# Kernel optimization log

Measured on AMD Instinct MI355X. Metric: run time of the kernel, lower is better.

## Reference

```python
import jax, jax.numpy as jnp
import numpy as np

EPSILON = 0.3
ALPHA = 0.7
LN_EPS = 1e-5


def _layernorm(x, g, b):
    mu = jnp.mean(x, axis=-1, keepdims=True)
    var = jnp.mean((x - mu) ** 2, axis=-1, keepdims=True)
    return (x - mu) / jnp.sqrt(var + LN_EPS) * g + b


def setup_inputs() -> dict:
    key = jax.random.key(0)
    ks = jax.random.split(key, 6)
    B, N, D, L = 1, 2048, 768, 16
    s = 0.05  # weight scale to keep sigmoid/exp well-conditioned
    return {
        "x": jax.random.normal(ks[0], (B, N, D), jnp.float32),
        "proj_w": jax.random.normal(ks[1], (D, L), jnp.float32) * s,
        "proj_b": jnp.zeros((L,), jnp.float32),
        "ln1_g": jnp.ones((L,), jnp.float32),
        "ln1_b": jnp.zeros((L,), jnp.float32),
        "pi_w1": jax.random.normal(ks[2], (L, D), jnp.float32) * s,
        "pi_b1": jnp.zeros((D,), jnp.float32),
        "pi_w2": jax.random.normal(ks[3], (D, 1), jnp.float32) * s,
        "pi_b2": jnp.zeros((1,), jnp.float32),
        "dt": jnp.full((1,), 0.05, jnp.float32),
        "f_w": jax.random.normal(ks[4], (D, D), jnp.float32) * s,
        "f_b": jnp.zeros((D,), jnp.float32),
        "ln2_g": jnp.ones((D,), jnp.float32),
        "ln2_b": jnp.zeros((D,), jnp.float32),
    }


def reference(x, proj_w, proj_b, ln1_g, ln1_b, pi_w1, pi_b1, pi_w2, pi_b2, dt, f_w, f_b, ln2_g, ln2_b):
    B, N, D = x.shape
    # proj_list: Linear -> LayerNorm -> ReLU. [B,N,L]
    x_proj = jax.nn.relu(_layernorm(x @ proj_w + proj_b, ln1_g, ln1_b))
    # RBF kernel over pairwise differences. [B,N,N]
    diff = x_proj[:, :, None, :] - x_proj[:, None, :, :]
    K_eps = jnp.exp(-(1.0 / (4.0 * EPSILON)) * jnp.sum(diff * diff, axis=-1))
    q_tilde = jnp.sum(K_eps, axis=2)  # [B,N]
    # pi_list: Linear -> ReLU -> Linear -> Sigmoid. [B,N]
    pi = jax.nn.sigmoid(jax.nn.relu(x_proj @ pi_w1 + pi_b1) @ pi_w2 + pi_b2)[..., 0]
    v = pi / q_tilde  # diagonal of D_epsilon_tilde
    # K_tilde = K_eps @ diag(v): column scaling (math-equivalent to bmm with diag_embed)
    K_tilde = K_eps * v[:, None, :]
    d = jnp.sum(K_tilde, axis=2) + 1e-5  # diagonal of D_tilde
    # inv(D_tilde) @ K_tilde: row scaling; then subtract identity
    L_op = (1.0 / EPSILON) * (K_tilde / d[:, :, None]) - jnp.eye(N, dtype=x.dtype)[None]
    L_mat = L_op[0]  # .squeeze(0), B == 1
    # f(x): modeled as linear map
    target = x @ f_w + f_b  # [B,N,D]
    tt = dt * jnp.einsum('ij,bjd->bid', L_mat, target)  # target_transformed
    target1 = target + tt
    target2 = ALPHA * x + (1.0 - ALPHA) * (target1 + tt)
    return _layernorm(target2, ln2_g, ln2_b)
```

## Files before the change

kernel.cpp:

```cpp
#include <hip/hip_runtime.h>
#include <math.h>

#define EPSILON 0.3f
#define ALPHA 0.7f
#define LN_EPS 1e-5f

typedef __bf16 bf16x8 __attribute__((ext_vector_type(8)));
typedef float f32x4 __attribute__((ext_vector_type(4)));

__device__ __forceinline__ unsigned short f2bf(float f) {
  unsigned int u = __float_as_uint(f);
  return (unsigned short)((u + 0x7fffu + ((u >> 16) & 1u)) >> 16);
}
__device__ __forceinline__ float bf2f(unsigned short h) {
  return __uint_as_float(((unsigned int)h) << 16);
}
__device__ __forceinline__ unsigned int pack2(float lo, float hi) {
  return (unsigned int)f2bf(lo) | ((unsigned int)f2bf(hi) << 16);
}

__device__ __forceinline__ void async16(const unsigned short* g,
                                        unsigned short* l) {
  __builtin_amdgcn_global_load_lds(
      (const __attribute__((address_space(1))) unsigned int*)g,
      (__attribute__((address_space(3))) unsigned int*)l, 16, 0, 0);
}

__device__ __forceinline__ float wave_reduce(float v) {
#pragma unroll
  for (int off = 32; off > 0; off >>= 1) v += __shfl_xor(v, off, 64);
  return v;
}

__device__ __forceinline__ float blk_reduce_sum(float v, float* red) {
  v = wave_reduce(v);
  int lane = threadIdx.x & 63, wid = threadIdx.x >> 6;
  __syncthreads();
  if (lane == 0) red[wid] = v;
  __syncthreads();
  return red[0] + red[1] + red[2] + red[3];
}

__global__ __launch_bounds__(256) void k_proj(
    const float* __restrict__ x, const float* __restrict__ proj_w,
    const float* __restrict__ proj_b, const float* __restrict__ ln1_g,
    const float* __restrict__ ln1_b, const float* __restrict__ pi_w1,
    const float* __restrict__ pi_b1, const float* __restrict__ pi_w2,
    const float* __restrict__ pi_b2, const float* __restrict__ fw,
    unsigned short* __restrict__ fwTb, float* __restrict__ xp,
    float* __restrict__ s, float* __restrict__ pi, int N, int D) {
  __shared__ float xs[16][68];
  __shared__ float ws[64][20];
  __shared__ float ysh[16][17];
  __shared__ float xps[16][16];
  __shared__ float pr[16][4];
  int tid = threadIdx.x;
  int nProj = N / 16;
  if (blockIdx.x >= (unsigned)nProj) {
    unsigned short(*tile)[33] = (unsigned short(*)[33])&ws[0][0];
    int t = blockIdx.x - nProj;
    int tx = tid & 31, ty = tid >> 5;
    int cols = D / 32;
    int c0 = (t % cols) * 32, r0 = (t / cols) * 32;
#pragma unroll
    for (int i = 0; i < 4; ++i) {
      int r = r0 + ty + i * 8;
      tile[ty + i * 8][tx] = f2bf(fw[(size_t)r * D + c0 + tx]);
    }
    __syncthreads();
#pragma unroll
    for (int i = 0; i < 4; ++i) {
      int cc = c0 + ty + i * 8;
      fwTb[(size_t)cc * D + r0 + tx] = tile[tx][ty + i * 8];
    }
    return;
  }
  int row0 = blockIdx.x * 16;
  int row = tid >> 4, l = tid & 15;
  int lane = tid & 63, w = tid >> 6;
  int skc = (tid & 15) * 4;
  int wk = tid >> 2, wl = (tid & 3) * 4;
  float acc = 0.f;
  for (int k0 = 0; k0 < D; k0 += 64) {
    float4 xv = *(const float4*)(x + (size_t)(row0 + row) * D + k0 + skc);
    float4 wv = *(const float4*)(proj_w + (size_t)(k0 + wk) * 16 + wl);
    __syncthreads();
    *(float4*)&xs[row][skc] = xv;
    *(float4*)&ws[wk][wl] = wv;
    __syncthreads();
#pragma unroll
    for (int kk = 0; kk < 64; kk += 4) {
      float4 a4 = *(const float4*)&xs[row][kk];
      acc += a4.x * ws[kk + 0][l];
      acc += a4.y * ws[kk + 1][l];
      acc += a4.z * ws[kk + 2][l];
      acc += a4.w * ws[kk + 3][l];
    }
  }
  float y = acc + proj_b[l];
  ysh[row][l] = y;
  __syncthreads();
  float mu = 0.f;
#pragma unroll
  for (int t = 0; t < 16; ++t) mu += ysh[row][t];
  mu *= (1.f / 16.f);
  float var = 0.f;
#pragma unroll
  for (int t = 0; t < 16; ++t) { float d2 = ysh[row][t] - mu; var += d2 * d2; }
  var *= (1.f / 16.f);
  float rstd = rsqrtf(var + LN_EPS);
  float xpv = fmaxf((y - mu) * rstd * ln1_g[l] + ln1_b[l], 0.f);
  xps[row][l] = xpv;
  xp[(size_t)(row0 + row) * 16 + l] = xpv;
  float sq = xpv * xpv;
  sq += __shfl_xor(sq, 8, 64);
  sq += __shfl_xor(sq, 4, 64);
  sq += __shfl_xor(sq, 2, 64);
  sq += __shfl_xor(sq, 1, 64);
  if ((lane & 15) == 0) s[row0 + row] = sq;
  __syncthreads();
  float w1r[3][16], b1r[3], w2r[3];
#pragma unroll
  for (int c = 0; c < 3; ++c) {
    int d0 = tid + c * 256;
    b1r[c] = pi_b1[d0];
    w2r[c] = pi_w2[d0];
#pragma unroll
    for (int t = 0; t < 16; ++t) w1r[c][t] = pi_w1[(size_t)t * D + d0];
  }
#pragma unroll
  for (int r = 0; r < 16; ++r) {
    float xv[16];
#pragma unroll
    for (int t4 = 0; t4 < 4; ++t4) {
      float4 xq = *(const float4*)&xps[r][t4 * 4];
      xv[t4 * 4 + 0] = xq.x; xv[t4 * 4 + 1] = xq.y;
      xv[t4 * 4 + 2] = xq.z; xv[t4 * 4 + 3] = xq.w;
    }
    float pa = 0.f;
#pragma unroll
    for (int c = 0; c < 3; ++c) {
      float h = b1r[c];
#pragma unroll
      for (int t = 0; t < 16; ++t) h += xv[t] * w1r[c][t];
      h = fmaxf(h, 0.f);
      pa += h * w2r[c];
    }
    float pv = wave_reduce(pa);
    if (lane == 0) pr[r][w] = pv;
  }
  __syncthreads();
  if (tid < 16) {
    float tot = pr[tid][0] + pr[tid][1] + pr[tid][2] + pr[tid][3] + pi_b2[0];
    pi[row0 + tid] = 1.f / (1.f + expf(-tot));
  }
}

__global__ __launch_bounds__(256) void k_keps(
    const float* __restrict__ xp, const float* __restrict__ s,
    const float* __restrict__ pi, unsigned short* __restrict__ Kb,
    unsigned short* __restrict__ vb, int N) {
  __shared__ float qs[4][4];
  int i0 = blockIdx.x * 4;
  int tid = threadIdx.x, lane = tid & 63, w = tid >> 6;
  float a[4][16], si[4];
#pragma unroll
  for (int r = 0; r < 4; ++r) {
    const float* ap = xp + (size_t)(i0 + r) * 16;
#pragma unroll
    for (int t = 0; t < 16; ++t) a[r][t] = ap[t];
    si[r] = s[i0 + r];
  }
  const float c = 1.f / (4.f * EPSILON);
  float qa[4] = {0.f, 0.f, 0.f, 0.f};
  for (int it = 0; it < N / 512; ++it) {
    int j = it * 512 + tid * 2;
    const float4* bp = (const float4*)(xp + (size_t)j * 16);
    float4 b0 = bp[0], b1 = bp[1], b2 = bp[2], b3 = bp[3];
    float4 c0 = bp[4], c1 = bp[5], c2 = bp[6], c3 = bp[7];
    float bv[16] = {b0.x, b0.y, b0.z, b0.w, b1.x, b1.y, b1.z, b1.w,
                    b2.x, b2.y, b2.z, b2.w, b3.x, b3.y, b3.z, b3.w};
    float cv[16] = {c0.x, c0.y, c0.z, c0.w, c1.x, c1.y, c1.z, c1.w,
                    c2.x, c2.y, c2.z, c2.w, c3.x, c3.y, c3.z, c3.w};
    float sj0 = s[j], sj1 = s[j + 1];
#pragma unroll
    for (int r = 0; r < 4; ++r) {
      float d0 = 0.f, d1 = 0.f;
#pragma unroll
      for (int t = 0; t < 16; ++t) { d0 += a[r][t] * bv[t]; d1 += a[r][t] * cv[t]; }
      float k0 = __expf(-c * (si[r] + sj0 - 2.f * d0));
      float k1 = __expf(-c * (si[r] + sj1 - 2.f * d1));
      *(unsigned int*)(Kb + (size_t)(i0 + r) * N + j) = pack2(k0, k1);
      qa[r] += k0 + k1;
    }
  }
#pragma unroll
  for (int r = 0; r < 4; ++r) {
    float t = wave_reduce(qa[r]);
    if (lane == 0) qs[r][w] = t;
  }
  __syncthreads();
  if (tid < 4) {
    float tot = qs[tid][0] + qs[tid][1] + qs[tid][2] + qs[tid][3];
    vb[i0 + tid] = f2bf(pi[i0 + tid] / tot);
  }
}

__global__ __launch_bounds__(256) void k_scale(
    const float* __restrict__ x, const unsigned short* __restrict__ vb,
    unsigned short* __restrict__ xvbT, int N, int D) {
  __shared__ unsigned short tile[32][33];
  int tid = threadIdx.x;
  int tx = tid & 31, ty = tid >> 5;
  int cols = D / 32;
  int c0 = ((int)blockIdx.x % cols) * 32;
  int r0 = ((int)blockIdx.x / cols) * 32;
#pragma unroll
  for (int i = 0; i < 4; ++i) {
    int r = r0 + ty + i * 8;
    tile[ty + i * 8][tx] = f2bf(bf2f(vb[r]) * x[(size_t)r * D + c0 + tx]);
  }
  __syncthreads();
#pragma unroll
  for (int i = 0; i < 4; ++i) {
    int cc = c0 + ty + i * 8;
    xvbT[(size_t)cc * N + r0 + tx] = tile[tx][ty + i * 8];
  }
}

__global__ __launch_bounds__(256) void k_gemmA(
    const unsigned short* __restrict__ A, const unsigned short* __restrict__ Bt,
    const unsigned short* __restrict__ vb, const float* __restrict__ x,
    const float* __restrict__ dtp, unsigned short* __restrict__ Z,
    int M, int N, int K) {
  __shared__ unsigned short As[64 * 64];
  __shared__ unsigned short Bs[64 * 64];
  int tid = threadIdx.x;
  int w = tid >> 6, l = tid & 63;
  int ln = l & 15, quad = l >> 4;
  int mh = (w & 1) * 32, nh = (w >> 1) * 32;
  int row0 = blockIdx.y * 64, col0 = blockIdx.x * 64;
  int sr = l >> 3, sj = l & 7;
  int swz = (sj ^ sr) * 8;
  const unsigned short* gA0 = A + (size_t)(row0 + w * 8 + sr) * K + swz;
  const unsigned short* gB0 = Bt + (size_t)(col0 + w * 8 + sr) * K + swz;
  const unsigned short* gA1 = gA0 + (size_t)32 * K;
  const unsigned short* gB1 = gB0 + (size_t)32 * K;
  f32x4 acc[2][2] = {};
  f32x4 adv[2] = {};
  for (int k0 = 0; k0 < K; k0 += 64) {
    __syncthreads();
    async16(gA0 + k0, As + w * 8 * 64);
    async16(gA1 + k0, As + (32 + w * 8) * 64);
    async16(gB0 + k0, Bs + w * 8 * 64);
    async16(gB1 + k0, Bs + (32 + w * 8) * 64);
    __syncthreads();
#pragma unroll
    for (int ks = 0; ks < 2; ++ks) {
      bf16x8 bfr[2], afr[2];
      bf16x8 bvf = *(const bf16x8*)(vb + k0 + ks * 32 + quad * 8);
#pragma unroll
      for (int nt = 0; nt < 2; ++nt) {
        int r = nh + nt * 16 + ln;
        int cix = (ks * 4 + quad) ^ (r & 7);
        bfr[nt] = *(const bf16x8*)&Bs[r * 64 + cix * 8];
      }
#pragma unroll
      for (int mt = 0; mt < 2; ++mt) {
        int r = mh + mt * 16 + ln;
        int cix = (ks * 4 + quad) ^ (r & 7);
        afr[mt] = *(const bf16x8*)&As[r * 64 + cix * 8];
      }
#pragma unroll
      for (int mt = 0; mt < 2; ++mt) {
        adv[mt] = __builtin_amdgcn_mfma_f32_16x16x32_bf16(afr[mt], bvf,
                                                          adv[mt], 0, 0, 0);
#pragma unroll
        for (int nt = 0; nt < 2; ++nt)
          acc[mt][nt] = __builtin_amdgcn_mfma_f32_16x16x32_bf16(
              afr[mt], bfr[nt], acc[mt][nt], 0, 0, 0);
      }
    }
  }
  float dtv = dtp[0];
  float c2 = (1.f - ALPHA) * (1.f - 2.f * dtv);
  float c3b = (1.f - ALPHA) * 2.f * dtv / EPSILON;
#pragma unroll
  for (int mt = 0; mt < 2; ++mt)
#pragma unroll
    for (int nt = 0; nt < 2; ++nt) {
      int col = col0 + nh + nt * 16 + ln;
#pragma unroll
      for (int r = 0; r < 4; ++r) {
        int row = row0 + mh + mt * 16 + quad * 4 + r;
        float dvv = adv[mt][r] + 1e-5f;
        Z[(size_t)row * N + col] =
            f2bf(c2 * x[(size_t)row * N + col] + (c3b / dvv) * acc[mt][nt][r]);
      }
    }
}

__global__ __launch_bounds__(256) void k_gemmB(
    const unsigned short* __restrict__ A, const unsigned short* __restrict__ Bt,
    const float* __restrict__ x, const float* __restrict__ bias,
    const float* __restrict__ dtp, float* __restrict__ out,
    int M, int N, int K) {
  __shared__ unsigned short As[64 * 64];
  __shared__ unsigned short Bs[64 * 64];
  int tid = threadIdx.x;
  int w = tid >> 6, l = tid & 63;
  int ln = l & 15, quad = l >> 4;
  int mh = (w & 1) * 32, nh = (w >> 1) * 32;
  int row0 = blockIdx.y * 64, col0 = blockIdx.x * 64;
  int sr = l >> 3, sj = l & 7;
  int swz = (sj ^ sr) * 8;
  const unsigned short* gA0 = A + (size_t)(row0 + w * 8 + sr) * K + swz;
  const unsigned short* gB0 = Bt + (size_t)(col0 + w * 8 + sr) * K + swz;
  const unsigned short* gA1 = gA0 + (size_t)32 * K;
  const unsigned short* gB1 = gB0 + (size_t)32 * K;
  f32x4 acc[2][2] = {};
  for (int k0 = 0; k0 < K; k0 += 64) {
    __syncthreads();
    async16(gA0 + k0, As + w * 8 * 64);
    async16(gA1 + k0, As + (32 + w * 8) * 64);
    async16(gB0 + k0, Bs + w * 8 * 64);
    async16(gB1 + k0, Bs + (32 + w * 8) * 64);
    __syncthreads();
#pragma unroll
    for (int ks = 0; ks < 2; ++ks) {
      bf16x8 bfr[2], afr[2];
#pragma unroll
      for (int nt = 0; nt < 2; ++nt) {
        int r = nh + nt * 16 + ln;
        int cix = (ks * 4 + quad) ^ (r & 7);
        bfr[nt] = *(const bf16x8*)&Bs[r * 64 + cix * 8];
      }
#pragma unroll
      for (int mt = 0; mt < 2; ++mt) {
        int r = mh + mt * 16 + ln;
        int cix = (ks * 4 + quad) ^ (r & 7);
        afr[mt] = *(const bf16x8*)&As[r * 64 + cix * 8];
      }
#pragma unroll
      for (int mt = 0; mt < 2; ++mt)
#pragma unroll
        for (int nt = 0; nt < 2; ++nt)
          acc[mt][nt] = __builtin_amdgcn_mfma_f32_16x16x32_bf16(
              afr[mt], bfr[nt], acc[mt][nt], 0, 0, 0);
    }
  }
  float dtv = dtp[0];
  float cb = (1.f - ALPHA) * (1.f - 2.f * dtv) +
             (1.f - ALPHA) * 2.f * dtv / EPSILON;
#pragma unroll
  for (int mt = 0; mt < 2; ++mt)
#pragma unroll
    for (int nt = 0; nt < 2; ++nt) {
      int col = col0 + nh + nt * 16 + ln;
      float bv = cb * bias[col];
#pragma unroll
      for (int r = 0; r < 4; ++r) {
        int row = row0 + mh + mt * 16 + quad * 4 + r;
        size_t idx = (size_t)row * N + col;
        out[idx] = ALPHA * x[idx] + acc[mt][nt][r] + bv;
      }
    }
}

__global__ __launch_bounds__(256) void k_ln_rows(
    float* __restrict__ out, const float* __restrict__ g,
    const float* __restrict__ b, int D) {
  __shared__ float red[4];
  int i = blockIdx.x, tid = threadIdx.x;
  float vv[4];
  int nt = D / 256;
  float sum = 0.f;
  for (int t = 0; t < nt; ++t) {
    vv[t] = out[(size_t)i * D + tid + t * 256];
    sum += vv[t];
  }
  float mu = blk_reduce_sum(sum, red) / (float)D;
  float sq = 0.f;
  for (int t = 0; t < nt; ++t) { float d2 = vv[t] - mu; sq += d2 * d2; }
  float var = blk_reduce_sum(sq, red) / (float)D;
  float rs = rsqrtf(var + LN_EPS);
  for (int t = 0; t < nt; ++t) {
    int d0 = tid + t * 256;
    out[(size_t)i * D + d0] = (vv[t] - mu) * rs * g[d0] + b[d0];
  }
}

extern "C" void kernel_launch(void* const* d_in, const int* in_sizes, int n_in,
                              void* d_out, int out_size, void* d_ws, size_t ws_size,
                              hipStream_t stream) {
  const float* x = (const float*)d_in[0];
  const float* proj_w = (const float*)d_in[1];
  const float* proj_b = (const float*)d_in[2];
  const float* ln1_g = (const float*)d_in[3];
  const float* ln1_b = (const float*)d_in[4];
  const float* pi_w1 = (const float*)d_in[5];
  const float* pi_b1 = (const float*)d_in[6];
  const float* pi_w2 = (const float*)d_in[7];
  const float* pi_b2 = (const float*)d_in[8];
  const float* dt = (const float*)d_in[9];
  const float* f_w = (const float*)d_in[10];
  const float* f_b = (const float*)d_in[11];
  const float* ln2_g = (const float*)d_in[12];
  const float* ln2_b = (const float*)d_in[13];
  float* out = (float*)d_out;

  int D = in_sizes[11];
  int N = in_sizes[0] / D;

  unsigned short* Kb = (unsigned short*)d_ws;
  unsigned short* xvbT = Kb + (size_t)N * N;
  unsigned short* fwTb = xvbT + (size_t)D * N;
  unsigned short* Z = fwTb + (size_t)D * D;
  unsigned short* vb = Z + (size_t)N * D;
  float* xp = (float*)(vb + N);
  float* s = xp + (size_t)N * 16;
  float* pi = s + N;

  int fwB = (D / 32) * (D / 32);

  k_proj<<<N / 16 + fwB, 256, 0, stream>>>(x, proj_w, proj_b, ln1_g, ln1_b,
                                           pi_w1, pi_b1, pi_w2, pi_b2, f_w,
                                           fwTb, xp, s, pi, N, D);
  k_keps<<<N / 4, 256, 0, stream>>>(xp, s, pi, Kb, vb, N);
  k_scale<<<(N / 32) * (D / 32), 256, 0, stream>>>(x, vb, xvbT, N, D);
  k_gemmA<<<dim3(D / 64, N / 64), 256, 0, stream>>>(Kb, xvbT, vb, x, dt, Z,
                                                    N, D, N);
  k_gemmB<<<dim3(D / 64, N / 64), 256, 0, stream>>>(Z, fwTb, x, f_b, dt, out,
                                                    N, D, D);
  k_ln_rows<<<N, 256, 0, stream>>>(out, ln2_g, ln2_b, D);
}
```

Before: 171.9 us.

## Fuse all stages into one persistent kernel with atomic grid barriers

Replaces the six separate kernel launches with a single persistent kernel of 256 blocks. Each stage walks its tiles in a grid-stride loop, and stages are separated by a software grid barrier built on atomic counters. The row-sum d of K_tilde now appears to be computed in its own stage into a dv buffer instead of by an extra MFMA inside gemmA, and v is kept in fp32. This removes launch gaps and the tail effects between kernels, but it caps parallelism at 256 blocks and adds spin-wait barrier cost, with a deadlock risk if not all blocks are co-resident.

```diff
diff --git a/kernel.cpp b/kernel.cpp
--- a/kernel.cpp
+++ b/kernel.cpp
@@ -4,6 +4,7 @@
 #define EPSILON 0.3f
 #define ALPHA 0.7f
 #define LN_EPS 1e-5f
+#define NBLK 256
 
 typedef __bf16 bf16x8 __attribute__((ext_vector_type(8)));
 typedef float f32x4 __attribute__((ext_vector_type(4)));
@@ -11,9 +12,6 @@
 __device__ __forceinline__ unsigned short f2bf(float f) {
   unsigned int u = __float_as_uint(f);
   return (unsigned short)((u + 0x7fffu + ((u >> 16) & 1u)) >> 16);
-}
-__device__ __forceinline__ float bf2f(unsigned short h) {
-  return __uint_as_float(((unsigned int)h) << 16);
 }
 __device__ __forceinline__ unsigned int pack2(float lo, float hi) {
   return (unsigned int)f2bf(lo) | ((unsigned int)f2bf(hi) << 16);
@@ -41,396 +39,451 @@
   return red[0] + red[1] + red[2] + red[3];
 }
 
-__global__ __launch_bounds__(256) void k_proj(
-    const float* __restrict__ x, const float* __restrict__ proj_w,
-    const float* __restrict__ proj_b, const float* __restrict__ ln1_g,
-    const float* __restrict__ ln1_b, const float* __restrict__ pi_w1,
-    const float* __restrict__ pi_b1, const float* __restrict__ pi_w2,
-    const float* __restrict__ pi_b2, const float* __restrict__ fw,
-    unsigned short* __restrict__ fwTb, float* __restrict__ xp,
-    float* __restrict__ s, float* __restrict__ pi, int N, int D) {
-  __shared__ float xs[16][68];
-  __shared__ float ws[64][20];
-  __shared__ float ysh[16][17];
-  __shared__ float xps[16][16];
-  __shared__ float pr[16][4];
-  int tid = threadIdx.x;
-  int nProj = N / 16;
-  if (blockIdx.x >= (unsigned)nProj) {
-    unsigned short(*tile)[33] = (unsigned short(*)[33])&ws[0][0];
-    int t = blockIdx.x - nProj;
-    int tx = tid & 31, ty = tid >> 5;
-    int cols = D / 32;
-    int c0 = (t % cols) * 32, r0 = (t / cols) * 32;
-#pragma unroll
-    for (int i = 0; i < 4; ++i) {
-      int r = r0 + ty + i * 8;
-      tile[ty + i * 8][tx] = f2bf(fw[(size_t)r * D + c0 + tx]);
-    }
-    __syncthreads();
-#pragma unroll
-    for (int i = 0; i < 4; ++i) {
-      int cc = c0 + ty + i * 8;
-      fwTb[(size_t)cc * D + r0 + tx] = tile[tx][ty + i * 8];
-    }
-    return;
-  }
-  int row0 = blockIdx.x * 16;
-  int row = tid >> 4, l = tid & 15;
-  int lane = tid & 63, w = tid >> 6;
-  int skc = (tid & 15) * 4;
-  int wk = tid >> 2, wl = (tid & 3) * 4;
-  float acc = 0.f;
-  for (int k0 = 0; k0 < D; k0 += 64) {
-    float4 xv = *(const float4*)(x + (size_t)(row0 + row) * D + k0 + skc);
-    float4 wv = *(const float4*)(proj_w + (size_t)(k0 + wk) * 16 + wl);
-    __syncthreads();
-    *(float4*)&xs[row][skc] = xv;
-    *(float4*)&ws[wk][wl] = wv;
-    __syncthreads();
-#pragma unroll
-    for (int kk = 0; kk < 64; kk += 4) {
-      float4 a4 = *(const float4*)&xs[row][kk];
-      acc += a4.x * ws[kk + 0][l];
-      acc += a4.y * ws[kk + 1][l];
-      acc += a4.z * ws[kk + 2][l];
-      acc += a4.w * ws[kk + 3][l];
-    }
-  }
-  float y = acc + proj_b[l];
-  ysh[row][l] = y;
+__device__ __forceinline__ void gbar(unsigned* bar, int idx) {
   __syncthreads();
-  float mu = 0.f;
-#pragma unroll
-  for (int t = 0; t < 16; ++t) mu += ysh[row][t];
-  mu *= (1.f / 16.f);
-  float var = 0.f;
-#pragma unroll
-  for (int t = 0; t < 16; ++t) { float d2 = ysh[row][t] - mu; var += d2 * d2; }
-  var *= (1.f / 16.f);
-  float rstd = rsqrtf(var + LN_EPS);
-  float xpv = fmaxf((y - mu) * rstd * ln1_g[l] + ln1_b[l], 0.f);
-  xps[row][l] = xpv;
-  xp[(size_t)(row0 + row) * 16 + l] = xpv;
-  float sq = xpv * xpv;
-  sq += __shfl_xor(sq, 8, 64);
-  sq += __shfl_xor(sq, 4, 64);
-  sq += __shfl_xor(sq, 2, 64);
-  sq += __shfl_xor(sq, 1, 64);
-  if ((lane & 15) == 0) s[row0 + row] = sq;
+  if (threadIdx.x == 0) {
+    __threadfence();
+    atomicAdd(&bar[idx], 1u);
+    while (atomicAdd(&bar[idx], 0u) < NBLK) __builtin_amdgcn_s_sleep(16);
+    __threadfence();
+  }
   __syncthreads();
-  float w1r[3][16], b1r[3], w2r[3];
-#pragma unroll
-  for (int c = 0; c < 3; ++c) {
-    int d0 = tid + c * 256;
-    b1r[c] = pi_b1[d0];
-    w2r[c] = pi_w2[d0];
-#pragma unroll
-    for (int t = 0; t < 16; ++t) w1r[c][t] = pi_w1[(size_t)t * D + d0];
-  }
-#pragma unroll
-  for (int r = 0; r < 16; ++r) {
-    float xv[16];
-#pragma unroll
-    for (int t4 = 0; t4 < 4; ++t4) {
-      float4 xq = *(const float4*)&xps[r][t4 * 4];
-      xv[t4 * 4 + 0] = xq.x; xv[t4 * 4 + 1] = xq.y;
-      xv[t4 * 4 + 2] = xq.z; xv[t4 * 4 + 3] = xq.w;
-    }
-    float pa = 0.f;
-#pragma unroll
-    for (int c = 0; c < 3; ++c) {
-      float h = b1r[c];
-#pragma unroll
-      for (int t = 0; t < 16; ++t) h += xv[t] * w1r[c][t];
-      h = fmaxf(h, 0.f);
-      pa += h * w2r[c];
-    }
-    float pv = wave_reduce(pa);
-    if (lane == 0) pr[r][w] = pv;
-  }
-  __syncthreads();
-  if (tid < 16) {
-    float tot = pr[tid][0] + pr[tid][1] + pr[tid][2] + pr[tid][3] + pi_b2[0];
-    pi[row0 + tid] = 1.f / (1.f + expf(-tot));
-  }
-}
-
-__global__ __launch_bounds__(256) void k_keps(
-    const float* __restrict__ xp, const float* __restrict__ s,
-    const float* __restrict__ pi, unsigned short* __restrict__ Kb,
-    unsigned short* __restrict__ vb, int N) {
-  __shared__ float qs[4][4];
-  int i0 = blockIdx.x * 4;
-  int tid = threadIdx.x, lane = tid & 63, w = tid >> 6;
-  float a[4][16], si[4];
-#pragma unroll
-  for (int r = 0; r < 4; ++r) {
-    const float* ap = xp + (size_t)(i0 + r) * 16;
-#pragma unroll
-    for (int t = 0; t < 16; ++t) a[r][t] = ap[t];
-    si[r] = s[i0 + r];
-  }
-  const float c = 1.f / (4.f * EPSILON);
-  float qa[4] = {0.f, 0.f, 0.f, 0.f};
-  for (int it = 0; it < N / 512; ++it) {
-    int j = it * 512 + tid * 2;
-    const float4* bp = (const float4*)(xp + (size_t)j * 16);
-    float4 b0 = bp[0], b1 = bp[1], b2 = bp[2], b3 = bp[3];
-    float4 c0 = bp[4], c1 = bp[5], c2 = bp[6], c3 = bp[7];
-    float bv[16] = {b0.x, b0.y, b0.z, b0.w, b1.x, b1.y, b1.z, b1.w,
-                    b2.x, b2.y, b2.z, b2.w, b3.x, b3.y, b3.z, b3.w};
-    float cv[16] = {c0.x, c0.y, c0.z, c0.w, c1.x, c1.y, c1.z, c1.w,
-                    c2.x, c2.y, c2.z, c2.w, c3.x, c3.y, c3.z, c3.w};
-    float sj0 = s[j], sj1 = s[j + 1];
-#pragma unroll
-    for (int r = 0; r < 4; ++r) {
-      float d0 = 0.f, d1 = 0.f;
-#pragma unroll
-      for (int t = 0; t < 16; ++t) { d0 += a[r][t] * bv[t]; d1 += a[r][t] * cv[t]; }
-      float k0 = __expf(-c * (si[r] + sj0 - 2.f * d0));
-      float k1 = __expf(-c * (si[r] + sj1 - 2.f * d1));
-      *(unsigned int*)(Kb + (size_t)(i0 + r) * N + j) = pack2(k0, k1);
-      qa[r] += k0 + k1;
-    }
-  }
-#pragma unroll
-  for (int r = 0; r < 4; ++r) {
-    float t = wave_reduce(qa[r]);
-    if (lane == 0) qs[r][w] = t;
-  }
-  __syncthreads();
-  if (tid < 4) {
-    float tot = qs[tid][0] + qs[tid][1] + qs[tid][2] + qs[tid][3];
-    vb[i0 + tid] = f2bf(pi[i0 + tid] / tot);
-  }
-}
-
-__global__ __launch_bounds__(256) void k_scale(
-    const float* __restrict__ x, const unsigned short* __restrict__ vb,
-    unsigned short* __restrict__ xvbT, int N, int D) {
-  __shared__ unsigned short tile[32][33];
-  int tid = threadIdx.x;
-  int tx = tid & 31, ty = tid >> 5;
-  int cols = D / 32;
-  int c0 = ((int)blockIdx.x % cols) * 32;
-  int r0 = ((int)blockIdx.x / cols) * 32;
-#pragma unroll
-  for (int i = 0; i < 4; ++i) {
-    int r = r0 + ty + i * 8;
-    tile[ty + i * 8][tx] = f2bf(bf2f(vb[r]) * x[(size_t)r * D + c0 + tx]);
-  }
-  __syncthreads();
-#pragma unroll
-  for (int i = 0; i < 4; ++i) {
-    int cc = c0 + ty + i * 8;
-    xvbT[(size_t)cc * N + r0 + tx] = tile[tx][ty + i * 8];
-  }
-}
-
-__global__ __launch_bounds__(256) void k_gemmA(
-    const unsigned short* __restrict__ A, const unsigned short* __restrict__ Bt,
-    const unsigned short* __restrict__ vb, const float* __restrict__ x,
-    const float* __restrict__ dtp, unsigned short* __restrict__ Z,
-    int M, int N, int K) {
-  __shared__ unsigned short As[64 * 64];
-  __shared__ unsigned short Bs[64 * 64];
-  int tid = threadIdx.x;
-  int w = tid >> 6, l = tid & 63;
-  int ln = l & 15, quad = l >> 4;
-  int mh = (w & 1) * 32, nh = (w >> 1) * 32;
-  int row0 = blockIdx.y * 64, col0 = blockIdx.x * 64;
-  int sr = l >> 3, sj = l & 7;
-  int swz = (sj ^ sr) * 8;
-  const unsigned short* gA0 = A + (size_t)(row0 + w * 8 + sr) * K + swz;
-  const unsigned short* gB0 = Bt + (size_t)(col0 + w * 8 + sr) * K + swz;
-  const unsigned short* gA1 = gA0 + (size_t)32 * K;
-  const unsigned short* gB1 = gB0 + (size_t)32 * K;
-  f32x4 acc[2][2] = {};
-  f32x4 adv[2] = {};
-  for (int k0 = 0; k0 < K; k0 += 64) {
-    __syncthreads();
-    async16(gA0 + k0, As + w * 8 * 64);
-    async16(gA1 + k0, As + (32 + w * 8) * 64);
-    async16(gB0 + k0, Bs + w * 8 * 64);
-    async16(gB1 + k0, Bs + (32 + w * 8) * 64);
-    __syncthreads();
-#pragma unroll
-    for (int ks = 0; ks < 2; ++ks) {
-      bf16x8 bfr[2], afr[2];
-      bf16x8 bvf = *(const bf16x8*)(vb + k0 + ks * 32 + quad * 8);
-#pragma unroll
-      for (int nt = 0; nt < 2; ++nt) {
-        int r = nh + nt * 16 + ln;
-        int cix = (ks * 4 + quad) ^ (r & 7);
-        bfr[nt] = *(const bf16x8*)&Bs[r * 64 + cix * 8];
-      }
-#pragma unroll
-      for (int mt = 0; mt < 2; ++mt) {
-        int r = mh + mt * 16 + ln;
-        int cix = (ks * 4 + quad) ^ (r & 7);
-        afr[mt] = *(const bf16x8*)&As[r * 64 + cix * 8];
-      }
-#pragma unroll
-      for (int mt = 0; mt < 2; ++mt) {
-        adv[mt] = __builtin_amdgcn_mfma_f32_16x16x32_bf16(afr[mt], bvf,
-                                                          adv[mt], 0, 0, 0);
-#pragma unroll
-        for (int nt = 0; nt < 2; ++nt)
-          acc[mt][nt] = __builtin_amdgcn_mfma_f32_16x16x32_bf16(
-              afr[mt], bfr[nt], acc[mt][nt], 0, 0, 0);
-      }
-    }
-  }
-  float dtv = dtp[0];
-  float c2 = (1.f - ALPHA) * (1.f - 2.f * dtv);
-  float c3b = (1.f - ALPHA) * 2.f * dtv / EPSILON;
-#pragma unroll
-  for (int mt = 0; mt < 2; ++mt)
-#pragma unroll
-    for (int nt = 0; nt < 2; ++nt) {
-      int col = col0 + nh + nt * 16 + ln;
+}
+
+struct Prm {
+  const float *x, *proj_w, *proj_b, *ln1_g, *ln1_b, *pi_w1, *pi_b1, *pi_w2,
+      *pi_b2, *dt, *f_w, *f_b, *ln2_g, *ln2_b;
+  float* out;
+  unsigned short *Kb, *xvbT, *fwTb, *Z;
+  float *xp, *s, *pi, *v, *dv;
+  unsigned* bar;
+  int N, D;
+};
+
+__global__ __launch_bounds__(256, 2) void k_mega(Prm p) {
+  __shared__ __align__(16) char smem[16384];
+  const int tid = threadIdx.x;
+  const int bid = blockIdx.x;
+  const int N = p.N, D = p.D;
+
+  {
+    const int nProj = N / 16;
+    const int dc = D / 32;
+    const int fwB = dc * dc;
+    float* xs = (float*)smem;
+    float* wsm = xs + 16 * 68;
+    float* ysh = wsm + 64 * 20;
+    float* xps = ysh + 16 * 17;
+    float* pr = xps + 16 * 16;
+    unsigned short(*tile)[33] = (unsigned short(*)[33])smem;
+    for (int t = bid; t < nProj + fwB; t += NBLK) {
+      __syncthreads();
+      if (t < nProj) {
+        int row0 = t * 16;
+        int row = tid >> 4, l = tid & 15;
+        int lane = tid & 63, w = tid >> 6;
+        int skc = (tid & 15) * 4;
+        int wk = tid >> 2, wl = (tid & 3) * 4;
+        float acc = 0.f;
+        for (int k0 = 0; k0 < D; k0 += 64) {
+          float4 xv = *(const float4*)(p.x + (size_t)(row0 + row) * D + k0 + skc);
+          float4 wv = *(const float4*)(p.proj_w + (size_t)(k0 + wk) * 16 + wl);
+          __syncthreads();
+          *(float4*)&xs[row * 68 + skc] = xv;
+          *(float4*)&wsm[wk * 20 + wl] = wv;
+          __syncthreads();
+#pragma unroll
+          for (int kk = 0; kk < 64; kk += 4) {
+            float4 a4 = *(const float4*)&xs[row * 68 + kk];
+            acc += a4.x * wsm[(kk + 0) * 20 + l];
+            acc += a4.y * wsm[(kk + 1) * 20 + l];
+            acc += a4.z * wsm[(kk + 2) * 20 + l];
+            acc += a4.w * wsm[(kk + 3) * 20 + l];
+          }
+        }
+        float y = acc + p.proj_b[l];
+        ysh[row * 17 + l] = y;
+        __syncthreads();
+        float mu = 0.f;
+#pragma unroll
+        for (int u = 0; u < 16; ++u) mu += ysh[row * 17 + u];
+        mu *= (1.f / 16.f);
+        float var = 0.f;
+#pragma unroll
+        for (int u = 0; u < 16; ++u) {
+          float d2 = ysh[row * 17 + u] - mu;
+          var += d2 * d2;
+        }
+        var *= (1.f / 16.f);
+        float rstd = rsqrtf(var + LN_EPS);
+        float xpv = fmaxf((y - mu) * rstd * p.ln1_g[l] + p.ln1_b[l], 0.f);
+        xps[row * 16 + l] = xpv;
+        p.xp[(size_t)(row0 + row) * 16 + l] = xpv;
+        float sq = xpv * xpv;
+        sq += __shfl_xor(sq, 8, 64);
+        sq += __shfl_xor(sq, 4, 64);
+        sq += __shfl_xor(sq, 2, 64);
+        sq += __shfl_xor(sq, 1, 64);
+        if ((lane & 15) == 0) p.s[row0 + row] = sq;
+        __syncthreads();
+        float w1r[3][16], b1r[3], w2r[3];
+#pragma unroll
+        for (int c = 0; c < 3; ++c) {
+          int d0 = tid + c * 256;
+          b1r[c] = p.pi_b1[d0];
+          w2r[c] = p.pi_w2[d0];
+#pragma unroll
+          for (int u = 0; u < 16; ++u) w1r[c][u] = p.pi_w1[(size_t)u * D + d0];
+        }
+#pragma unroll
+        for (int r = 0; r < 16; ++r) {
+          float xv[16];
+#pragma unroll
+          for (int t4 = 0; t4 < 4; ++t4) {
+            float4 xq = *(const float4*)&xps[r * 16 + t4 * 4];
+            xv[t4 * 4 + 0] = xq.x; xv[t4 * 4 + 1] = xq.y;
+            xv[t4 * 4 + 2] = xq.z; xv[t4 * 4 + 3] = xq.w;
+          }
+          float pa = 0.f;
+#pragma unroll
+          for (int c = 0; c < 3; ++c) {
+            float h = b1r[c];
+#pragma unroll
+            for (int u = 0; u < 16; ++u) h += xv[u] * w1r[c][u];
+            h = fmaxf(h, 0.f);
+            pa += h * w2r[c];
+          }
+          float pv = wave_reduce(pa);
+          if (lane == 0) pr[r * 4 + w] = pv;
+        }
+        __syncthreads();
+        if (tid < 16) {
+          float tot = pr[tid * 4] + pr[tid * 4 + 1] + pr[tid * 4 + 2] +
+                      pr[tid * 4 + 3] + p.pi_b2[0];
+          p.pi[t * 16 + tid] = 1.f / (1.f + expf(-tot));
+        }
+      } else {
+        int t2 = t - nProj;
+        int tx = tid & 31, ty = tid >> 5;
+        int c0 = (t2 % dc) * 32, r0 = (t2 / dc) * 32;
+#pragma unroll
+        for (int i = 0; i < 4; ++i) {
+          int r = r0 + ty + i * 8;
+          tile[ty + i * 8][tx] = f2bf(p.f_w[(size_t)r * D + c0 + tx]);
+        }
+        __syncthreads();
+#pragma unroll
+        for (int i = 0; i < 4; ++i) {
+          int cc = c0 + ty + i * 8;
+          p.fwTb[(size_t)cc * D + r0 + tx] = tile[tx][ty + i * 8];
+        }
+      }
+    }
+  }
+  gbar(p.bar, 0);
+
+  {
+    float* qs = (float*)smem;
+    int lane = tid & 63, w = tid >> 6;
+    const float c = 1.f / (4.f * EPSILON);
+    for (int t = bid; t < N / 4; t += NBLK) {
+      int i0 = t * 4;
+      float a[4][16], si[4];
 #pragma unroll
       for (int r = 0; r < 4; ++r) {
-        int row = row0 + mh + mt * 16 + quad * 4 + r;
-        float dvv = adv[mt][r] + 1e-5f;
-        Z[(size_t)row * N + col] =
-            f2bf(c2 * x[(size_t)row * N + col] + (c3b / dvv) * acc[mt][nt][r]);
-      }
-    }
-}
-
-__global__ __launch_bounds__(256) void k_gemmB(
-    const unsigned short* __restrict__ A, const unsigned short* __restrict__ Bt,
-    const float* __restrict__ x, const float* __restrict__ bias,
-    const float* __restrict__ dtp, float* __restrict__ out,
-    int M, int N, int K) {
-  __shared__ unsigned short As[64 * 64];
-  __shared__ unsigned short Bs[64 * 64];
-  int tid = threadIdx.x;
-  int w = tid >> 6, l = tid & 63;
-  int ln = l & 15, quad = l >> 4;
-  int mh = (w & 1) * 32, nh = (w >> 1) * 32;
-  int row0 = blockIdx.y * 64, col0 = blockIdx.x * 64;
-  int sr = l >> 3, sj = l & 7;
-  int swz = (sj ^ sr) * 8;
-  const unsigned short* gA0 = A + (size_t)(row0 + w * 8 + sr) * K + swz;
-  const unsigned short* gB0 = Bt + (size_t)(col0 + w * 8 + sr) * K + swz;
-  const unsigned short* gA1 = gA0 + (size_t)32 * K;
-  const unsigned short* gB1 = gB0 + (size_t)32 * K;
-  f32x4 acc[2][2] = {};
-  for (int k0 = 0; k0 < K; k0 += 64) {
-    __syncthreads();
-    async16(gA0 + k0, As + w * 8 * 64);
-    async16(gA1 + k0, As + (32 + w * 8) * 64);
-    async16(gB0 + k0, Bs + w * 8 * 64);
-    async16(gB1 + k0, Bs + (32 + w * 8) * 64);
-    __syncthreads();
-#pragma unroll
-    for (int ks = 0; ks < 2; ++ks) {
-      bf16x8 bfr[2], afr[2];
-#pragma unroll
-      for (int nt = 0; nt < 2; ++nt) {
-        int r = nh + nt * 16 + ln;
-        int cix = (ks * 4 + quad) ^ (r & 7);
-        bfr[nt] = *(const bf16x8*)&Bs[r * 64 + cix * 8];
-      }
-#pragma unroll
-      for (int mt = 0; mt < 2; ++mt) {
-        int r = mh + mt * 16 + ln;
-        int cix = (ks * 4 + quad) ^ (r & 7);
-        afr[mt] = *(const bf16x8*)&As[r * 64 + cix * 8];
+        const float* ap = p.xp + (size_t)(i0 + r) * 16;
+#pragma unroll
+        for (int u = 0; u < 16; ++u) a[r][u] = ap[u];
+        si[r] = p.s[i0 + r];
+      }
+      float qa[4] = {0.f, 0.f, 0.f, 0.f};
+      for (int it = 0; it < N / 512; ++it) {
+        int j = it * 512 + tid * 2;
+        const float4* bp = (const float4*)(p.xp + (size_t)j * 16);
+        float4 b0 = bp[0], b1 = bp[1], b2 = bp[2], b3 = bp[3];
+        float4 c0 = bp[4], c1 = bp[5], c2 = bp[6], c3 = bp[7];
+        float bv[16] = {b0.x, b0.y, b0.z, b0.w, b1.x, b1.y, b1.z, b1.w,
+                        b2.x, b2.y, b2.z, b2.w, b3.x, b3.y, b3.z, b3.w};
+        float cv[16] = {c0.x, c0.y, c0.z, c0.w, c1.x, c1.y, c1.z, c1.w,
+                        c2.x, c2.y, c2.z, c2.w, c3.x, c3.y, c3.z, c3.w};
+        float sj0 = p.s[j], sj1 = p.s[j + 1];
+#pragma unroll
+        for (int r = 0; r < 4; ++r) {
+          float d0 = 0.f, d1 = 0.f;
+#pragma unroll
+          for (int u = 0; u < 16; ++u) {
+            d0 += a[r][u] * bv[u];
+            d1 += a[r][u] * cv[u];
+          }
+          float k0 = __expf(-c * (si[r] + sj0 - 2.f * d0));
+          float k1 = __expf(-c * (si[r] + sj1 - 2.f * d1));
+          *(unsigned int*)(p.Kb + (size_t)(i0 + r) * N + j) = pack2(k0, k1);
+          qa[r] += k0 + k1;
+        }
+      }
+      __syncthreads();
+#pragma unroll
+      for (int r = 0; r < 4; ++r) {
+        float tt = wave_reduce(qa[r]);
+        if (lane == 0) qs[r * 4 + w] = tt;
+      }
+      __syncthreads();
+      if (tid < 4) {
+        float tot = qs[tid * 4] + qs[tid * 4 + 1] + qs[tid * 4 + 2] +
+                    qs[tid * 4 + 3];
+        p.v[i0 + tid] = p.pi[i0 + tid] / tot;
+      }
+    }
+  }
+  gbar(p.bar, 1);
+
+  {
+    const int dc = D / 32;
+    const int xvB = (N / 32) * dc;
+    float* red = (float*)smem;
+    unsigned short(*tile)[33] = (unsigned short(*)[33])smem;
+    for (int t = bid; t < N + xvB; t += NBLK) {
+      __syncthreads();
+      if (t < N) {
+        float acc = 0.f;
+        for (int j8 = tid * 8; j8 < N; j8 += 256 * 8) {
+          uint4 kv4 = *(const uint4*)(p.Kb + (size_t)t * N + j8);
+          float4 va = *(const float4*)(p.v + j8);
+          float4 vb2 = *(const float4*)(p.v + j8 + 4);
+          unsigned int u;
+          u = kv4.x;
+          acc += __uint_as_float(u << 16) * va.x +
+                 __uint_as_float(u & 0xffff0000u) * va.y;
+          u = kv4.y;
+          acc += __uint_as_float(u << 16) * va.z +
+                 __uint_as_float(u & 0xffff0000u) * va.w;
+          u = kv4.z;
+          acc += __uint_as_float(u << 16) * vb2.x +
+                 __uint_as_float(u & 0xffff0000u) * vb2.y;
+          u = kv4.w;
+          acc += __uint_as_float(u << 16) * vb2.z +
+                 __uint_as_float(u & 0xffff0000u) * vb2.w;
+        }
+        float tot = blk_reduce_sum(acc, red);
+        if (tid == 0) p.dv[t] = tot + 1e-5f;
+      } else {
+        int t3 = t - N;
+        int tx = tid & 31, ty = tid >> 5;
+        int c0 = (t3 % dc) * 32;
+        int r0 = (t3 / dc) * 32;
+#pragma unroll
+        for (int i = 0; i < 4; ++i) {
+          int r = r0 + ty + i * 8;
+          tile[ty + i * 8][tx] = f2bf(p.v[r] * p.x[(size_t)r * D + c0 + tx]);
+        }
+        __syncthreads();
+#pragma unroll
+        for (int i = 0; i < 4; ++i) {
+          int cc = c0 + ty + i * 8;
+          p.xvbT[(size_t)cc * N + r0 + tx] = tile[tx][ty + i * 8];
+        }
+      }
+    }
+  }
+  gbar(p.bar, 2);
+
+  {
+    unsigned short* As = (unsigned short*)smem;
+    unsigned short* Bs = As + 64 * 64;
+    int w = tid >> 6, l = tid & 63;
+    int ln = l & 15, quad = l >> 4;
+    int mh = (w & 1) * 32, nh = (w >> 1) * 32;
+    int sr = l >> 3, sj = l & 7;
+    int swz = (sj ^ sr) * 8;
+    int ntile = (N / 64) * (D / 64);
+    float dtv = p.dt[0];
+    float c2 = (1.f - ALPHA) * (1.f - 2.f * dtv);
+    float c3b = (1.f - ALPHA) * 2.f * dtv / EPSILON;
+    for (int t = bid; t < ntile; t += NBLK) {
+      int row0 = (t / (D / 64)) * 64;
+      int col0 = (t % (D / 64)) * 64;
+      const unsigned short* gA0 = p.Kb + (size_t)(row0 + w * 8 + sr) * N + swz;
+      const unsigned short* gB0 = p.xvbT + (size_t)(col0 + w * 8 + sr) * N + swz;
+      const unsigned short* gA1 = gA0 + (size_t)32 * N;
+      const unsigned short* gB1 = gB0 + (size_t)32 * N;
+      f32x4 acc[2][2] = {};
+      for (int k0 = 0; k0 < N; k0 += 64) {
+        __syncthreads();
+        async16(gA0 + k0, As + w * 8 * 64);
+        async16(gA1 + k0, As + (32 + w * 8) * 64);
+        async16(gB0 + k0, Bs + w * 8 * 64);
+        async16(gB1 + k0, Bs + (32 + w * 8) * 64);
+        __syncthreads();
+#pragma unroll
+        for (int ks = 0; ks < 2; ++ks) {
+          bf16x8 bfr[2], afr[2];
+#pragma unroll
+          for (int nt = 0; nt < 2; ++nt) {
+            int r = nh + nt * 16 + ln;
+            int cix = (ks * 4 + quad) ^ (r & 7);
+            bfr[nt] = *(const bf16x8*)&Bs[r * 64 + cix * 8];
+          }
+#pragma unroll
+          for (int mt = 0; mt < 2; ++mt) {
+            int r = mh + mt * 16 + ln;
+            int cix = (ks * 4 + quad) ^ (r & 7);
+            afr[mt] = *(const bf16x8*)&As[r * 64 + cix * 8];
+          }
+#pragma unroll
+          for (int mt = 0; mt < 2; ++mt)
+#pragma unroll
+            for (int nt = 0; nt < 2; ++nt)
+              acc[mt][nt] = __builtin_amdgcn_mfma_f32_16x16x32_bf16(
+                  afr[mt], bfr[nt], acc[mt][nt], 0, 0, 0);
+        }
       }
 #pragma unroll
       for (int mt = 0; mt < 2; ++mt)
 #pragma unroll
-        for (int nt = 0; nt < 2; ++nt)
-          acc[mt][nt] = __builtin_amdgcn_mfma_f32_16x16x32_bf16(
-              afr[mt], bfr[nt], acc[mt][nt], 0, 0, 0);
-    }
-  }
-  float dtv = dtp[0];
-  float cb = (1.f - ALPHA) * (1.f - 2.f * dtv) +
-             (1.f - ALPHA) * 2.f * dtv / EPSILON;
-#pragma unroll
-  for (int mt = 0; mt < 2; ++mt)
-#pragma unroll
-    for (int nt = 0; nt < 2; ++nt) {
-      int col = col0 + nh + nt * 16 + ln;
-      float bv = cb * bias[col];
-#pragma unroll
-      for (int r = 0; r < 4; ++r) {
-        int row = row0 + mh + mt * 16 + quad * 4 + r;
-        size_t idx = (size_t)row * N + col;
-        out[idx] = ALPHA * x[idx] + acc[mt][nt][r] + bv;
-      }
-    }
-}
-
-__global__ __launch_bounds__(256) void k_ln_rows(
-    float* __restrict__ out, const float* __restrict__ g,
-    const float* __restrict__ b, int D) {
-  __shared__ float red[4];
-  int i = blockIdx.x, tid = threadIdx.x;
-  float vv[4];
-  int nt = D / 256;
-  float sum = 0.f;
-  for (int t = 0; t < nt; ++t) {
-    vv[t] = out[(size_t)i * D + tid + t * 256];
-    sum += vv[t];
-  }
-  float mu = blk_reduce_sum(sum, red) / (float)D;
-  float sq = 0.f;
-  for (int t = 0; t < nt; ++t) { float d2 = vv[t] - mu; sq += d2 * d2; }
-  float var = blk_reduce_sum(sq, red) / (float)D;
-  float rs = rsqrtf(var + LN_EPS);
-  for (int t = 0; t < nt; ++t) {
-    int d0 = tid + t * 256;
-    out[(size_t)i * D + d0] = (vv[t] - mu) * rs * g[d0] + b[d0];
+        for (int nt = 0; nt < 2; ++nt) {
+          int col = col0 + nh + nt * 16 + ln;
+#pragma unroll
+          for (int r = 0; r < 4; ++r) {
+            int row = row0 + mh + mt * 16 + quad * 4 + r;
+            float c3 = c3b / p.dv[row];
+            p.Z[(size_t)row * D + col] = f2bf(
+                c2 * p.x[(size_t)row * D + col] + c3 * acc[mt][nt][r]);
+          }
+        }
+    }
+  }
+  gbar(p.bar, 3);
+
+  {
+    unsigned short* As = (unsigned short*)smem;
+    unsigned short* Bs = As + 64 * 64;
+    int w = tid >> 6, l = tid & 63;
+    int ln = l & 15, quad = l >> 4;
+    int mh = (w & 1) * 32, nh = (w >> 1) * 32;
+    int sr = l >> 3, sj = l & 7;
+    int swz = (sj ^ sr) * 8;
+    int ntile = (N / 64) * (D / 64);
+    float dtv = p.dt[0];
+    float cb = (1.f - ALPHA) * (1.f - 2.f * dtv) +
+               (1.f - ALPHA) * 2.f * dtv / EPSILON;
+    for (int t = bid; t < ntile; t += NBLK) {
+      int row0 = (t / (D / 64)) * 64;
+      int col0 = (t % (D / 64)) * 64;
+      const unsigned short* gA0 = p.Z + (size_t)(row0 + w * 8 + sr) * D + swz;
+      const unsigned short* gB0 = p.fwTb + (size_t)(col0 + w * 8 + sr) * D + swz;
+      const unsigned short* gA1 = gA0 + (size_t)32 * D;
+      const unsigned short* gB1 = gB0 + (size_t)32 * D;
+      f32x4 acc[2][2] = {};
+      for (int k0 = 0; k0 < D; k0 += 64) {
+        __syncthreads();
+        async16(gA0 + k0, As + w * 8 * 64);
+        async16(gA1 + k0, As + (32 + w * 8) * 64);
+        async16(gB0 + k0, Bs + w * 8 * 64);
+        async16(gB1 + k0, Bs + (32 + w * 8) * 64);
+        __syncthreads();
+#pragma unroll
+        for (int ks = 0; ks < 2; ++ks) {
+          bf16x8 bfr[2], afr[2];
+#pragma unroll
+          for (int nt = 0; nt < 2; ++nt) {
+            int r = nh + nt * 16 + ln;
+            int cix = (ks * 4 + quad) ^ (r & 7);
+            bfr[nt] = *(const bf16x8*)&Bs[r * 64 + cix * 8];
+          }
+#pragma unroll
+          for (int mt = 0; mt < 2; ++mt) {
+            int r = mh + mt * 16 + ln;
+            int cix = (ks * 4 + quad) ^ (r & 7);
+            afr[mt] = *(const bf16x8*)&As[r * 64 + cix * 8];
+          }
+#pragma unroll
+          for (int mt = 0; mt < 2; ++mt)
+#pragma unroll
+            for (int nt = 0; nt < 2; ++nt)
+              acc[mt][nt] = __builtin_amdgcn_mfma_f32_16x16x32_bf16(
+                  afr[mt], bfr[nt], acc[mt][nt], 0, 0, 0);
+        }
+      }
+#pragma unroll
+      for (int mt = 0; mt < 2; ++mt)
+#pragma unroll
+        for (int nt = 0; nt < 2; ++nt) {
+          int col = col0 + nh + nt * 16 + ln;
+          float bv = cb * p.f_b[col];
+#pragma unroll
+          for (int r = 0; r < 4; ++r) {
+            int row = row0 + mh + mt * 16 + quad * 4 + r;
+            size_t idx = (size_t)row * D + col;
+            p.out[idx] = ALPHA * p.x[idx] + acc[mt][nt][r] + bv;
+          }
+        }
+    }
+  }
+  gbar(p.bar, 4);
+
+  {
+    float* red = (float*)smem;
+    for (int t = bid; t < N; t += NBLK) {
+      float vv[4];
+      int nt = D / 256;
+      float sum = 0.f;
+      for (int u = 0; u < nt; ++u) {
+        vv[u] = p.out[(size_t)t * D + tid + u * 256];
+        sum += vv[u];
+      }
+      float mu = blk_reduce_sum(sum, red) / (float)D;
+      float sq = 0.f;
+      for (int u = 0; u < nt; ++u) {
+        float d2 = vv[u] - mu;
+        sq += d2 * d2;
+      }
+      float var = blk_reduce_sum(sq, red) / (float)D;
+      float rs = rsqrtf(var + LN_EPS);
+      for (int u = 0; u < nt; ++u) {
+        int d0 = tid + u * 256;
+        p.out[(size_t)t * D + d0] =
+            (vv[u] - mu) * rs * p.ln2_g[d0] + p.ln2_b[d0];
+      }
+    }
   }
 }
 
 extern "C" void kernel_launch(void* const* d_in, const int* in_sizes, int n_in,
                               void* d_out, int out_size, void* d_ws, size_t ws_size,
                               hipStream_t stream) {
-  const float* x = (const float*)d_in[0];
-  const float* proj_w = (const float*)d_in[1];
-  const float* proj_b = (const float*)d_in[2];
-  const float* ln1_g = (const float*)d_in[3];
-  const float* ln1_b = (const float*)d_in[4];
-  const float* pi_w1 = (const float*)d_in[5];
-  const float* pi_b1 = (const float*)d_in[6];
-  const float* pi_w2 = (const float*)d_in[7];
-  const float* pi_b2 = (const float*)d_in[8];
-  const float* dt = (const float*)d_in[9];
-  const float* f_w = (const float*)d_in[10];
-  const float* f_b = (const float*)d_in[11];
-  const float* ln2_g = (const float*)d_in[12];
-  const float* ln2_b = (const float*)d_in[13];
-  float* out = (float*)d_out;
+  Prm p;
+  p.x = (const float*)d_in[0];
+  p.proj_w = (const float*)d_in[1];
+  p.proj_b = (const float*)d_in[2];
+  p.ln1_g = (const float*)d_in[3];
+  p.ln1_b = (const float*)d_in[4];
+  p.pi_w1 = (const float*)d_in[5];
+  p.pi_b1 = (const float*)d_in[6];
+  p.pi_w2 = (const float*)d_in[7];
+  p.pi_b2 = (const float*)d_in[8];
+  p.dt = (const float*)d_in[9];
+  p.f_w = (const float*)d_in[10];
+  p.f_b = (const float*)d_in[11];
+  p.ln2_g = (const float*)d_in[12];
+  p.ln2_b = (const float*)d_in[13];
+  p.out = (float*)d_out;
 
   int D = in_sizes[11];
   int N = in_sizes[0] / D;
-
-  unsigned short* Kb = (unsigned short*)d_ws;
-  unsigned short* xvbT = Kb + (size_t)N * N;
-  unsigned short* fwTb = xvbT + (size_t)D * N;
-  unsigned short* Z = fwTb + (size_t)D * D;
-  unsigned short* vb = Z + (size_t)N * D;
-  float* xp = (float*)(vb + N);
-  float* s = xp + (size_t)N * 16;
-  float* pi = s + N;
-
-  int fwB = (D / 32) * (D / 32);
-
-  k_proj<<<N / 16 + fwB, 256, 0, stream>>>(x, proj_w, proj_b, ln1_g, ln1_b,
-                                           pi_w1, pi_b1, pi_w2, pi_b2, f_w,
-                                           fwTb, xp, s, pi, N, D);
-  k_keps<<<N / 4, 256, 0, stream>>>(xp, s, pi, Kb, vb, N);
-  k_scale<<<(N / 32) * (D / 32), 256, 0, stream>>>(x, vb, xvbT, N, D);
-  k_gemmA<<<dim3(D / 64, N / 64), 256, 0, stream>>>(Kb, xvbT, vb, x, dt, Z,
-                                                    N, D, N);
-  k_gemmB<<<dim3(D / 64, N / 64), 256, 0, stream>>>(Z, fwTb, x, f_b, dt, out,
-                                                    N, D, D);
-  k_ln_rows<<<N, 256, 0, stream>>>(out, ln2_g, ln2_b, D);
-}
+  p.N = N;
+  p.D = D;
+
+  p.Kb = (unsigned short*)d_ws;
+  p.xvbT = p.Kb + (size_t)N * N;
+  p.fwTb = p.xvbT + (size_t)D * N;
+  p.Z = p.fwTb + (size_t)D * D;
+  p.xp = (float*)(p.Z + (size_t)N * D);
+  p.s = p.xp + (size_t)N * 16;
+  p.pi = p.s + N;
+  p.v = p.pi + N;
+  p.dv = p.v + N;
+  p.bar = (unsigned*)(p.dv + N);
+
+  hipMemsetAsync(p.bar, 0, 8 * sizeof(unsigned), stream);
+  k_mega<<<NBLK, 256, 0, stream>>>(p);
+}
```

After: 303.4 us. +76.5%, slower.
